# Performance work log

Hardware: AMD Instinct MI355X
Metric: run time of the kernel (lower is better)

The kernel has to match this reference:

```python
import jax, jax.numpy as jnp
import numpy as np

N = 65536
APP = 1024
SP = 512
HID = 512
CARD = 16
SUB = HID // CARD  # 32


def setup_inputs() -> dict:
    key = jax.random.key(0)
    ks = jax.random.split(key, 8)
    s1 = 1.0 / np.sqrt(APP)
    s2 = 1.0 / np.sqrt(SP)
    s3 = 1.0 / np.sqrt(SUB)
    return {
        "appearance": jax.random.normal(ks[0], (N, APP), jnp.float32),
        "spatial": jax.random.normal(ks[1], (N, SP), jnp.float32),
        # Batched per-branch weights (torch Linear: y = x @ W.T + b; here stored as [in, out])
        "W1": jax.random.uniform(ks[2], (CARD, APP, SUB), jnp.float32, -s1, s1),
        "b1": jax.random.uniform(ks[3], (CARD, SUB), jnp.float32, -s1, s1),
        "W2": jax.random.uniform(ks[4], (CARD, SP, SUB), jnp.float32, -s2, s2),
        "b2": jax.random.uniform(ks[5], (CARD, SP if False else SUB), jnp.float32, -s2, s2),
        "W3": jax.random.uniform(ks[6], (CARD, SUB, HID), jnp.float32, -s3, s3),
        "b3": jax.random.uniform(ks[7], (CARD, HID), jnp.float32, -s3, s3),
    }


def reference(appearance, spatial, W1, b1, W2, b2, W3, b3):
    # fc1[c] = appearance @ W1[c] + b1[c]; fc2[c] = spatial @ W2[c] + b2[c]
    h1 = jnp.einsum('na,cas->ncs', appearance, W1) + b1[None]  # [N, C, SUB]
    h2 = jnp.einsum('np,cps->ncs', spatial, W2) + b2[None]     # [N, C, SUB]
    h = jax.nn.relu(h1 + h2)
    # sum over branches of (h[:,c] @ W3[c] + b3[c]) == einsum + sum of biases
    out = jnp.einsum('ncs,csh->nh', h, W3) + jnp.sum(b3, axis=0)[None]  # [N, HID]
    return jax.nn.relu(out)
```

## Files before the change

### kernel.cpp

```cpp
#include <hip/hip_runtime.h>

typedef __attribute__((ext_vector_type(4))) float floatx4;
typedef __attribute__((ext_vector_type(8))) short bf16x8;

__device__ __forceinline__ unsigned short f2bf(float f) {
    union { float f; unsigned u; } v; v.f = f;
    unsigned r = v.u + 0x7fffu + ((v.u >> 16) & 1u);
    return (unsigned short)(r >> 16);
}

__global__ void prep_kernel(const float* __restrict__ W1, const float* __restrict__ b1,
                            const float* __restrict__ W2, const float* __restrict__ b2,
                            const float* __restrict__ W3, const float* __restrict__ b3,
                            unsigned short* __restrict__ wcat, unsigned short* __restrict__ w3f,
                            float* __restrict__ bias12, float* __restrict__ bias3s)
{
    int tid = blockIdx.x * 256 + threadIdx.x;
    if (tid < 98304) {
        int l  = tid & 63;
        int nt = (tid >> 6) & 31;
        int kc = tid >> 11;
        int n  = nt * 16 + (l & 15);
        int k0 = kc * 32 + ((l >> 4) << 3);
        int c = n >> 5, s = n & 31;
        union { unsigned short us[8]; int4 v; } pk;
        const float* src = (k0 < 1024) ? (W1 + c * 32768 + k0 * 32 + s)
                                       : (W2 + c * 16384 + (k0 - 1024) * 32 + s);
        #pragma unroll
        for (int j = 0; j < 8; ++j) pk.us[j] = f2bf(src[j * 32]);
        *(int4*)(wcat + (size_t)tid * 8) = pk.v;
    } else if (tid < 131072) {
        int t  = tid - 98304;
        int l  = t & 63;
        int nt = (t >> 6) & 31;
        int kc = t >> 11;
        int n  = nt * 16 + (l & 15);
        int k0 = kc * 32 + ((l >> 4) << 3);
        union { unsigned short us[8]; int4 v; } pk;
        const float* src = W3 + k0 * 512 + n;
        #pragma unroll
        for (int j = 0; j < 8; ++j) pk.us[j] = f2bf(src[j * 512]);
        *(int4*)(w3f + (size_t)t * 8) = pk.v;
    } else if (tid < 131584) {
        int n = tid - 131072;
        bias12[n] = b1[n] + b2[n];
        float sacc = 0.f;
        #pragma unroll
        for (int c = 0; c < 16; ++c) sacc += b3[c * 512 + n];
        bias3s[n] = sacc;
    }
}

__global__ __launch_bounds__(512, 4) void fused_main(
    const float* __restrict__ app, const float* __restrict__ sp,
    const unsigned short* __restrict__ wcat, const unsigned short* __restrict__ w3f,
    const float* __restrict__ bias12, const float* __restrict__ bias3s,
    float* __restrict__ out)
{
    __shared__ union {
        unsigned short As[2][2][4][64][8];
        unsigned short Hf[4][16][64][8];
    } sh;

    const int tid = (int)threadIdx.x;
    const int w   = tid >> 6;
    const int l   = tid & 63;
    const int rowbase = (int)blockIdx.x * 64;

    const int sr = tid >> 3;
    const int kq = tid & 7;
    const float* appsrc = app + (size_t)(rowbase + sr) * 1024 + kq * 8;
    const float* spsrc  = sp  + (size_t)(rowbase + sr) * 512  + kq * 8;
    unsigned short* as0 = &sh.As[0][kq >> 2][sr >> 4][(kq & 3) * 16 + (sr & 15)][0];
    unsigned short* as1 = &sh.As[1][kq >> 2][sr >> 4][(kq & 3) * 16 + (sr & 15)][0];

    floatx4 acc[4][4];
    #pragma unroll
    for (int mt = 0; mt < 4; ++mt)
        #pragma unroll
        for (int nt = 0; nt < 4; ++nt)
            acc[mt][nt] = (floatx4){0.f, 0.f, 0.f, 0.f};

    const unsigned short* wbase = wcat + (size_t)w * 2048 + (size_t)l * 8;

    bf16x8 bcur[8];
    #pragma unroll
    for (int i = 0; i < 8; ++i)
        bcur[i] = *(const bf16x8*)(wbase + (i >> 2) * 16384 + (i & 3) * 512);
    {
        float4 q0 = *(const float4*)(appsrc);
        float4 q1 = *(const float4*)(appsrc + 4);
        union { unsigned short us[8]; int4 v; } pk;
        pk.us[0] = f2bf(q0.x); pk.us[1] = f2bf(q0.y); pk.us[2] = f2bf(q0.z); pk.us[3] = f2bf(q0.w);
        pk.us[4] = f2bf(q1.x); pk.us[5] = f2bf(q1.y); pk.us[6] = f2bf(q1.z); pk.us[7] = f2bf(q1.w);
        *(int4*)as0 = pk.v;
    }
    asm volatile("s_waitcnt lgkmcnt(0)" ::: "memory");
    __builtin_amdgcn_s_barrier();

    for (int p = 0; p < 24; ++p) {
        const int buf = p & 1;
        unsigned short* dst = buf ? as0 : as1;

        float4 pA0, pA1;
        if (p + 1 < 24) {
            const float* src = (p + 1 < 16) ? (appsrc + (p + 1) * 64)
                                            : (spsrc + (p - 15) * 64);
            pA0 = *(const float4*)src;
            pA1 = *(const float4*)(src + 4);
        }

        bf16x8 af[4];
        #pragma unroll
        for (int mt = 0; mt < 4; ++mt)
            af[mt] = *(const bf16x8*)(&sh.As[buf][0][mt][l][0]);
        __builtin_amdgcn_s_setprio(1);
        #pragma unroll
        for (int mt = 0; mt < 4; ++mt)
            #pragma unroll
            for (int nt = 0; nt < 4; ++nt)
                acc[mt][nt] = __builtin_amdgcn_mfma_f32_16x16x32_bf16(
                    af[mt], bcur[nt], acc[mt][nt], 0, 0, 0);
        __builtin_amdgcn_s_setprio(0);
        #pragma unroll
        for (int mt = 0; mt < 4; ++mt)
            af[mt] = *(const bf16x8*)(&sh.As[buf][1][mt][l][0]);
        __builtin_amdgcn_s_setprio(1);
        #pragma unroll
        for (int mt = 0; mt < 4; ++mt)
            #pragma unroll
            for (int nt = 0; nt < 4; ++nt)
                acc[mt][nt] = __builtin_amdgcn_mfma_f32_16x16x32_bf16(
                    af[mt], bcur[4 + nt], acc[mt][nt], 0, 0, 0);
        __builtin_amdgcn_s_setprio(0);

        if (p + 1 < 24) {
            const unsigned short* wp = wbase + (size_t)(p + 1) * 32768;
            #pragma unroll
            for (int i = 0; i < 8; ++i)
                bcur[i] = *(const bf16x8*)(wp + (i >> 2) * 16384 + (i & 3) * 512);
            union { unsigned short us[8]; int4 v; } pk;
            pk.us[0] = f2bf(pA0.x); pk.us[1] = f2bf(pA0.y); pk.us[2] = f2bf(pA0.z); pk.us[3] = f2bf(pA0.w);
            pk.us[4] = f2bf(pA1.x); pk.us[5] = f2bf(pA1.y); pk.us[6] = f2bf(pA1.z); pk.us[7] = f2bf(pA1.w);
            *(int4*)dst = pk.v;
        }

        asm volatile("s_waitcnt lgkmcnt(0)" ::: "memory");
        __builtin_amdgcn_s_barrier();
    }

    const unsigned short* w3base = w3f + (size_t)w * 2048 + (size_t)l * 8;
    bf16x8 b3[8];
    #pragma unroll
    for (int i = 0; i < 8; ++i)
        b3[i] = *(const bf16x8*)(w3base + (i >> 2) * 16384 + (i & 3) * 512);

    #pragma unroll
    for (int nt = 0; nt < 4; ++nt) {
        const int colg = w * 64 + nt * 16 + (l & 15);
        const float bv = bias12[colg];
        const int kc  = colg >> 5;
        const int lhi = ((colg >> 3) & 3) << 4;
        const int j   = colg & 7;
        #pragma unroll
        for (int mt = 0; mt < 4; ++mt)
            #pragma unroll
            for (int r = 0; r < 4; ++r) {
                const int rlow = ((l >> 4) << 2) + r;
                float v = acc[mt][nt][r] + bv;
                v = fmaxf(v, 0.f);
                sh.Hf[mt][kc][lhi + rlow][j] = f2bf(v);
            }
    }
    asm volatile("s_waitcnt lgkmcnt(0)" ::: "memory");
    __builtin_amdgcn_s_barrier();

    #pragma unroll
    for (int mt = 0; mt < 4; ++mt)
        #pragma unroll
        for (int nt = 0; nt < 4; ++nt)
            acc[mt][nt] = (floatx4){0.f, 0.f, 0.f, 0.f};

    for (int q = 0; q < 8; ++q) {
        bf16x8 af[4];
        #pragma unroll
        for (int mt = 0; mt < 4; ++mt)
            af[mt] = *(const bf16x8*)(&sh.Hf[mt][2 * q][l][0]);
        __builtin_amdgcn_s_setprio(1);
        #pragma unroll
        for (int mt = 0; mt < 4; ++mt)
            #pragma unroll
            for (int nt = 0; nt < 4; ++nt)
                acc[mt][nt] = __builtin_amdgcn_mfma_f32_16x16x32_bf16(
                    af[mt], b3[nt], acc[mt][nt], 0, 0, 0);
        __builtin_amdgcn_s_setprio(0);
        #pragma unroll
        for (int mt = 0; mt < 4; ++mt)
            af[mt] = *(const bf16x8*)(&sh.Hf[mt][2 * q + 1][l][0]);
        __builtin_amdgcn_s_setprio(1);
        #pragma unroll
        for (int mt = 0; mt < 4; ++mt)
            #pragma unroll
            for (int nt = 0; nt < 4; ++nt)
                acc[mt][nt] = __builtin_amdgcn_mfma_f32_16x16x32_bf16(
                    af[mt], b3[4 + nt], acc[mt][nt], 0, 0, 0);
        __builtin_amdgcn_s_setprio(0);
        if (q + 1 < 8) {
            const unsigned short* wp = w3base + (size_t)(q + 1) * 32768;
            #pragma unroll
            for (int i = 0; i < 8; ++i)
                b3[i] = *(const bf16x8*)(wp + (i >> 2) * 16384 + (i & 3) * 512);
        }
    }

    #pragma unroll
    for (int nt = 0; nt < 4; ++nt) {
        const int colg = w * 64 + nt * 16 + (l & 15);
        const float bv = bias3s[colg];
        #pragma unroll
        for (int mt = 0; mt < 4; ++mt)
            #pragma unroll
            for (int r = 0; r < 4; ++r) {
                const int rowg = mt * 16 + ((l >> 4) << 2) + r;
                float v = acc[mt][nt][r] + bv;
                v = fmaxf(v, 0.f);
                out[(size_t)(rowbase + rowg) * 512 + colg] = v;
            }
    }
}

extern "C" void kernel_launch(void* const* d_in, const int* in_sizes, int n_in,
                              void* d_out, int out_size, void* d_ws, size_t ws_size,
                              hipStream_t stream)
{
    const float* app = (const float*)d_in[0];
    const float* sp  = (const float*)d_in[1];
    const float* W1  = (const float*)d_in[2];
    const float* b1  = (const float*)d_in[3];
    const float* W2  = (const float*)d_in[4];
    const float* b2  = (const float*)d_in[5];
    const float* W3  = (const float*)d_in[6];
    const float* b3  = (const float*)d_in[7];

    char* ws = (char*)d_ws;
    unsigned short* wcat  = (unsigned short*)(ws);
    unsigned short* w3f   = (unsigned short*)(ws + 1572864);
    float*          b12   = (float*)(ws + 2097152);
    float*          b3s   = (float*)(ws + 2099200);

    prep_kernel<<<514, 256, 0, stream>>>(W1, b1, W2, b2, W3, b3, wcat, w3f, b12, b3s);

    float* outp = (float*)d_out;
    fused_main<<<65536 / 64, 512, 0, stream>>>(app, sp, wcat, w3f, b12, b3s, outp);
}
```

Measured before the change: 542.8 us.

## Swizzle LDS A tile, prefetch activations two stages ahead, split weight reloads

The bf16 activation tile in shared memory gets an XOR swizzle on both its write and read addresses to cut LDS bank conflicts. Global loads of the fp32 activations now run two pipeline stages ahead instead of one, so each load has a full iteration to arrive before conversion and store. Weight register reloads are split into two halves, each issued right after the MFMA block that last used those registers, so they overlap with the remaining compute. The change adds register pressure and depends on the swizzled write and read offsets matching the original layout exactly.

```diff
diff --git a/kernel.cpp b/kernel.cpp
--- a/kernel.cpp
+++ b/kernel.cpp
@@ -71,8 +71,20 @@
     const int kq = tid & 7;
     const float* appsrc = app + (size_t)(rowbase + sr) * 1024 + kq * 8;
     const float* spsrc  = sp  + (size_t)(rowbase + sr) * 512  + kq * 8;
-    unsigned short* as0 = &sh.As[0][kq >> 2][sr >> 4][(kq & 3) * 16 + (sr & 15)][0];
-    unsigned short* as1 = &sh.As[1][kq >> 2][sr >> 4][(kq & 3) * 16 + (sr & 15)][0];
+
+    {
+    }
+    const int halfw = kq >> 2, mtw = sr >> 4;
+    const int Lw    = ((kq & 3) << 4) + (sr & 15);
+    const int roww  = Lw >> 3, slotw = Lw & 7;
+    const int wroff = halfw * 4096 + mtw * 1024 + roww * 128 + ((slotw ^ roww) << 4);
+    char* shb = (char*)&sh;
+    unsigned short* as0 = (unsigned short*)(shb + wroff);
+    unsigned short* as1 = (unsigned short*)(shb + 8192 + wroff);
+
+    const int rdoff = ((l >> 3) << 7) + (((l & 7) ^ (l >> 3)) << 4);
+    #define AS_RD(buf, half, mt) \
+        (*(const bf16x8*)(shb + (buf) * 8192 + (half) * 4096 + (mt) * 1024 + rdoff))
 
     floatx4 acc[4][4];
     #pragma unroll
@@ -83,16 +95,18 @@
 
     const unsigned short* wbase = wcat + (size_t)w * 2048 + (size_t)l * 8;
 
+    float4 c00 = *(const float4*)(appsrc);
+    float4 c01 = *(const float4*)(appsrc + 4);
+    float4 pA0 = *(const float4*)(appsrc + 64);
+    float4 pA1 = *(const float4*)(appsrc + 68);
     bf16x8 bcur[8];
     #pragma unroll
     for (int i = 0; i < 8; ++i)
         bcur[i] = *(const bf16x8*)(wbase + (i >> 2) * 16384 + (i & 3) * 512);
     {
-        float4 q0 = *(const float4*)(appsrc);
-        float4 q1 = *(const float4*)(appsrc + 4);
         union { unsigned short us[8]; int4 v; } pk;
-        pk.us[0] = f2bf(q0.x); pk.us[1] = f2bf(q0.y); pk.us[2] = f2bf(q0.z); pk.us[3] = f2bf(q0.w);
-        pk.us[4] = f2bf(q1.x); pk.us[5] = f2bf(q1.y); pk.us[6] = f2bf(q1.z); pk.us[7] = f2bf(q1.w);
+        pk.us[0] = f2bf(c00.x); pk.us[1] = f2bf(c00.y); pk.us[2] = f2bf(c00.z); pk.us[3] = f2bf(c00.w);
+        pk.us[4] = f2bf(c01.x); pk.us[5] = f2bf(c01.y); pk.us[6] = f2bf(c01.z); pk.us[7] = f2bf(c01.w);
         *(int4*)as0 = pk.v;
     }
     asm volatile("s_waitcnt lgkmcnt(0)" ::: "memory");
@@ -100,49 +114,53 @@
 
     for (int p = 0; p < 24; ++p) {
         const int buf = p & 1;
-        unsigned short* dst = buf ? as0 : as1;
-
-        float4 pA0, pA1;
+
         if (p + 1 < 24) {
-            const float* src = (p + 1 < 16) ? (appsrc + (p + 1) * 64)
-                                            : (spsrc + (p - 15) * 64);
-            pA0 = *(const float4*)src;
-            pA1 = *(const float4*)(src + 4);
-        }
-
-        bf16x8 af[4];
-        #pragma unroll
-        for (int mt = 0; mt < 4; ++mt)
-            af[mt] = *(const bf16x8*)(&sh.As[buf][0][mt][l][0]);
-        __builtin_amdgcn_s_setprio(1);
-        #pragma unroll
-        for (int mt = 0; mt < 4; ++mt)
-            #pragma unroll
-            for (int nt = 0; nt < 4; ++nt)
-                acc[mt][nt] = __builtin_amdgcn_mfma_f32_16x16x32_bf16(
-                    af[mt], bcur[nt], acc[mt][nt], 0, 0, 0);
-        __builtin_amdgcn_s_setprio(0);
-        #pragma unroll
-        for (int mt = 0; mt < 4; ++mt)
-            af[mt] = *(const bf16x8*)(&sh.As[buf][1][mt][l][0]);
-        __builtin_amdgcn_s_setprio(1);
-        #pragma unroll
-        for (int mt = 0; mt < 4; ++mt)
-            #pragma unroll
-            for (int nt = 0; nt < 4; ++nt)
-                acc[mt][nt] = __builtin_amdgcn_mfma_f32_16x16x32_bf16(
-                    af[mt], bcur[4 + nt], acc[mt][nt], 0, 0, 0);
-        __builtin_amdgcn_s_setprio(0);
-
-        if (p + 1 < 24) {
-            const unsigned short* wp = wbase + (size_t)(p + 1) * 32768;
-            #pragma unroll
-            for (int i = 0; i < 8; ++i)
-                bcur[i] = *(const bf16x8*)(wp + (i >> 2) * 16384 + (i & 3) * 512);
             union { unsigned short us[8]; int4 v; } pk;
             pk.us[0] = f2bf(pA0.x); pk.us[1] = f2bf(pA0.y); pk.us[2] = f2bf(pA0.z); pk.us[3] = f2bf(pA0.w);
             pk.us[4] = f2bf(pA1.x); pk.us[5] = f2bf(pA1.y); pk.us[6] = f2bf(pA1.z); pk.us[7] = f2bf(pA1.w);
-            *(int4*)dst = pk.v;
+            *(int4*)((buf == 0) ? as1 : as0) = pk.v;
+        }
+        if (p + 2 < 24) {
+            const int c = p + 2;
+            const float* src = (c < 16) ? (appsrc + c * 64) : (spsrc + (c - 16) * 64);
+            pA0 = *(const float4*)src;
+            pA1 = *(const float4*)(src + 4);
+        }
+
+        bf16x8 af[4];
+        #pragma unroll
+        for (int mt = 0; mt < 4; ++mt)
+            af[mt] = AS_RD(buf, 0, mt);
+        __builtin_amdgcn_s_setprio(1);
+        #pragma unroll
+        for (int mt = 0; mt < 4; ++mt)
+            #pragma unroll
+            for (int nt = 0; nt < 4; ++nt)
+                acc[mt][nt] = __builtin_amdgcn_mfma_f32_16x16x32_bf16(
+                    af[mt], bcur[nt], acc[mt][nt], 0, 0, 0);
+        __builtin_amdgcn_s_setprio(0);
+        const unsigned short* wp = wbase + (size_t)(p + 1) * 32768;
+        if (p + 1 < 24) {
+            #pragma unroll
+            for (int i = 0; i < 4; ++i)
+                bcur[i] = *(const bf16x8*)(wp + i * 512);
+        }
+        #pragma unroll
+        for (int mt = 0; mt < 4; ++mt)
+            af[mt] = AS_RD(buf, 1, mt);
+        __builtin_amdgcn_s_setprio(1);
+        #pragma unroll
+        for (int mt = 0; mt < 4; ++mt)
+            #pragma unroll
+            for (int nt = 0; nt < 4; ++nt)
+                acc[mt][nt] = __builtin_amdgcn_mfma_f32_16x16x32_bf16(
+                    af[mt], bcur[4 + nt], acc[mt][nt], 0, 0, 0);
+        __builtin_amdgcn_s_setprio(0);
+        if (p + 1 < 24) {
+            #pragma unroll
+            for (int i = 0; i < 4; ++i)
+                bcur[4 + i] = *(const bf16x8*)(wp + 16384 + i * 512);
         }
 
         asm volatile("s_waitcnt lgkmcnt(0)" ::: "memory");
@@ -227,6 +245,7 @@
                 out[(size_t)(rowbase + rowg) * 512 + colg] = v;
             }
     }
+    #undef AS_RD
 }
 
 extern "C" void kernel_launch(void* const* d_in, const int* in_sizes, int n_in,
```

Result: slower. 634.5 us (+16.9%).

## Stream fp32 activations into LDS via direct global-to-LDS loads with triple buffering

Applied to the files above, without the earlier changes.

The register-staged global load, bf16 conversion and LDS store of the activation tile is replaced by global_load_lds DMA of raw fp32 into a three-deep LDS ring. Conversion to bf16 now happens after the LDS read, just before the MFMAs. The prefetch distance becomes two periods, with vmcnt-based waits instead of lgkmcnt. This frees VGPRs and removes the per-thread store path, at the cost of double the LDS read traffic and conversion work inside the compute loop, and it depends on correct vmcnt accounting.

```diff
diff --git a/kernel.cpp b/kernel.cpp
--- a/kernel.cpp
+++ b/kernel.cpp
@@ -1,4 +1,5 @@
 #include <hip/hip_runtime.h>
+#include <hip/hip_bf16.h>
 
 typedef __attribute__((ext_vector_type(4))) float floatx4;
 typedef __attribute__((ext_vector_type(8))) short bf16x8;
@@ -7,6 +8,21 @@
     union { float f; unsigned u; } v; v.f = f;
     unsigned r = v.u + 0x7fffu + ((v.u >> 16) & 1u);
     return (unsigned short)(r >> 16);
+}
+
+__device__ __forceinline__ bf16x8 cvt8(float4 lo, float4 hi) {
+    union { __hip_bfloat16 b[8]; bf16x8 v; } u;
+    u.b[0] = __float2bfloat16(lo.x); u.b[1] = __float2bfloat16(lo.y);
+    u.b[2] = __float2bfloat16(lo.z); u.b[3] = __float2bfloat16(lo.w);
+    u.b[4] = __float2bfloat16(hi.x); u.b[5] = __float2bfloat16(hi.y);
+    u.b[6] = __float2bfloat16(hi.z); u.b[7] = __float2bfloat16(hi.w);
+    return u.v;
+}
+
+__device__ __forceinline__ void dma16(const void* gsrc, void* ldst) {
+    __builtin_amdgcn_global_load_lds(
+        (const __attribute__((address_space(1))) unsigned*)gsrc,
+        (__attribute__((address_space(3))) unsigned*)ldst, 16, 0, 0);
 }
 
 __global__ void prep_kernel(const float* __restrict__ W1, const float* __restrict__ b1,
@@ -58,21 +74,68 @@
     float* __restrict__ out)
 {
     __shared__ union {
-        unsigned short As[2][2][4][64][8];
+        float          As32[3][8][2][64][4];
         unsigned short Hf[4][16][64][8];
     } sh;
+    char* shb = (char*)&sh;
 
     const int tid = (int)threadIdx.x;
     const int w   = tid >> 6;
     const int l   = tid & 63;
     const int rowbase = (int)blockIdx.x * 64;
 
-    const int sr = tid >> 3;
-    const int kq = tid & 7;
-    const float* appsrc = app + (size_t)(rowbase + sr) * 1024 + kq * 8;
-    const float* spsrc  = sp  + (size_t)(rowbase + sr) * 512  + kq * 8;
-    unsigned short* as0 = &sh.As[0][kq >> 2][sr >> 4][(kq & 3) * 16 + (sr & 15)][0];
-    unsigned short* as1 = &sh.As[1][kq >> 2][sr >> 4][(kq & 3) * 16 + (sr & 15)][0];
+    const int half = w >> 2, mtw = w & 3;
+    const int grow = rowbase + mtw * 16 + (l & 15);
+    const char* appB = (const char*)app + (size_t)grow * 4096 + half * 128 + (l >> 4) * 32;
+    const char* spB  = (const char*)sp  + (size_t)grow * 2048 + half * 128 + (l >> 4) * 32;
+
+    #define DMA_T(t) do {                                                     \
+        const char* _g = ((t) < 16) ? (appB + (t) * 256)                      \
+                                    : (spB + ((t) - 16) * 256);               \
+        char* _d = shb + ((t) % 3) * 16384 + w * 2048;                        \
+        dma16(_g,      _d);                                                   \
+        dma16(_g + 16, _d + 1024);                                            \
+    } while (0)
+
+    #define BLOAD(kp) do {                                                    \
+        const unsigned short* _wp = wbase + (size_t)(kp) * 32768;             \
+        _Pragma("unroll")                                                     \
+        for (int i = 0; i < 8; ++i)                                           \
+            bcur[i] = *(const bf16x8*)(_wp + (i >> 2) * 16384 + (i & 3) * 512);\
+    } while (0)
+
+    #define PERIOD_CORE(p) do {                                               \
+        const int _bo = ((p) % 3) * 16384;                                    \
+        bf16x8 af[4];                                                         \
+        _Pragma("unroll")                                                     \
+        for (int mt = 0; mt < 4; ++mt) {                                      \
+            float4 lo = *(const float4*)(shb + _bo + mt * 2048 + l * 16);     \
+            float4 hi = *(const float4*)(shb + _bo + mt * 2048 + 1024 + l * 16);\
+            af[mt] = cvt8(lo, hi);                                            \
+        }                                                                     \
+        __builtin_amdgcn_s_setprio(1);                                        \
+        _Pragma("unroll")                                                     \
+        for (int mt = 0; mt < 4; ++mt)                                        \
+            _Pragma("unroll")                                                 \
+            for (int nt = 0; nt < 4; ++nt)                                    \
+                acc[mt][nt] = __builtin_amdgcn_mfma_f32_16x16x32_bf16(        \
+                    af[mt], bcur[nt], acc[mt][nt], 0, 0, 0);                  \
+        __builtin_amdgcn_s_setprio(0);                                        \
+        _Pragma("unroll")                                                     \
+        for (int mt = 0; mt < 4; ++mt) {                                      \
+            float4 lo = *(const float4*)(shb + _bo + (4 + mt) * 2048 + l * 16);\
+            float4 hi = *(const float4*)(shb + _bo + (4 + mt) * 2048 + 1024 + l * 16);\
+            af[mt] = cvt8(lo, hi);                                            \
+        }                                                                     \
+        __builtin_amdgcn_s_setprio(1);                                        \
+        _Pragma("unroll")                                                     \
+        for (int mt = 0; mt < 4; ++mt)                                        \
+            _Pragma("unroll")                                                 \
+            for (int nt = 0; nt < 4; ++nt)                                    \
+                acc[mt][nt] = __builtin_amdgcn_mfma_f32_16x16x32_bf16(        \
+                    af[mt], bcur[4 + nt], acc[mt][nt], 0, 0, 0);              \
+        __builtin_amdgcn_s_setprio(0);                                        \
+    } while (0)
 
     floatx4 acc[4][4];
     #pragma unroll
@@ -84,70 +147,29 @@
     const unsigned short* wbase = wcat + (size_t)w * 2048 + (size_t)l * 8;
 
     bf16x8 bcur[8];
-    #pragma unroll
-    for (int i = 0; i < 8; ++i)
-        bcur[i] = *(const bf16x8*)(wbase + (i >> 2) * 16384 + (i & 3) * 512);
-    {
-        float4 q0 = *(const float4*)(appsrc);
-        float4 q1 = *(const float4*)(appsrc + 4);
-        union { unsigned short us[8]; int4 v; } pk;
-        pk.us[0] = f2bf(q0.x); pk.us[1] = f2bf(q0.y); pk.us[2] = f2bf(q0.z); pk.us[3] = f2bf(q0.w);
-        pk.us[4] = f2bf(q1.x); pk.us[5] = f2bf(q1.y); pk.us[6] = f2bf(q1.z); pk.us[7] = f2bf(q1.w);
-        *(int4*)as0 = pk.v;
-    }
-    asm volatile("s_waitcnt lgkmcnt(0)" ::: "memory");
-    __builtin_amdgcn_s_barrier();
-
-    for (int p = 0; p < 24; ++p) {
-        const int buf = p & 1;
-        unsigned short* dst = buf ? as0 : as1;
-
-        float4 pA0, pA1;
-        if (p + 1 < 24) {
-            const float* src = (p + 1 < 16) ? (appsrc + (p + 1) * 64)
-                                            : (spsrc + (p - 15) * 64);
-            pA0 = *(const float4*)src;
-            pA1 = *(const float4*)(src + 4);
-        }
-
-        bf16x8 af[4];
-        #pragma unroll
-        for (int mt = 0; mt < 4; ++mt)
-            af[mt] = *(const bf16x8*)(&sh.As[buf][0][mt][l][0]);
-        __builtin_amdgcn_s_setprio(1);
-        #pragma unroll
-        for (int mt = 0; mt < 4; ++mt)
-            #pragma unroll
-            for (int nt = 0; nt < 4; ++nt)
-                acc[mt][nt] = __builtin_amdgcn_mfma_f32_16x16x32_bf16(
-                    af[mt], bcur[nt], acc[mt][nt], 0, 0, 0);
-        __builtin_amdgcn_s_setprio(0);
-        #pragma unroll
-        for (int mt = 0; mt < 4; ++mt)
-            af[mt] = *(const bf16x8*)(&sh.As[buf][1][mt][l][0]);
-        __builtin_amdgcn_s_setprio(1);
-        #pragma unroll
-        for (int mt = 0; mt < 4; ++mt)
-            #pragma unroll
-            for (int nt = 0; nt < 4; ++nt)
-                acc[mt][nt] = __builtin_amdgcn_mfma_f32_16x16x32_bf16(
-                    af[mt], bcur[4 + nt], acc[mt][nt], 0, 0, 0);
-        __builtin_amdgcn_s_setprio(0);
-
-        if (p + 1 < 24) {
-            const unsigned short* wp = wbase + (size_t)(p + 1) * 32768;
-            #pragma unroll
-            for (int i = 0; i < 8; ++i)
-                bcur[i] = *(const bf16x8*)(wp + (i >> 2) * 16384 + (i & 3) * 512);
-            union { unsigned short us[8]; int4 v; } pk;
-            pk.us[0] = f2bf(pA0.x); pk.us[1] = f2bf(pA0.y); pk.us[2] = f2bf(pA0.z); pk.us[3] = f2bf(pA0.w);
-            pk.us[4] = f2bf(pA1.x); pk.us[5] = f2bf(pA1.y); pk.us[6] = f2bf(pA1.z); pk.us[7] = f2bf(pA1.w);
-            *(int4*)dst = pk.v;
-        }
-
-        asm volatile("s_waitcnt lgkmcnt(0)" ::: "memory");
+    BLOAD(0);
+    DMA_T(0);
+    DMA_T(1);
+    asm volatile("s_waitcnt vmcnt(2)" ::: "memory");
+    __builtin_amdgcn_s_barrier();
+    asm volatile("" ::: "memory");
+
+    for (int p = 0; p < 22; ++p) {
+        PERIOD_CORE(p);
+        BLOAD(p + 1);
+        DMA_T(p + 2);
+        asm volatile("s_waitcnt vmcnt(10)" ::: "memory");
         __builtin_amdgcn_s_barrier();
-    }
+        asm volatile("" ::: "memory");
+    }
+    PERIOD_CORE(22);
+    BLOAD(23);
+    asm volatile("s_waitcnt vmcnt(8)" ::: "memory");
+    __builtin_amdgcn_s_barrier();
+    asm volatile("" ::: "memory");
+    PERIOD_CORE(23);
+    __builtin_amdgcn_s_barrier();
+    asm volatile("" ::: "memory");
 
     const unsigned short* w3base = w3f + (size_t)w * 2048 + (size_t)l * 8;
     bf16x8 b3[8];
@@ -174,6 +196,7 @@
     }
     asm volatile("s_waitcnt lgkmcnt(0)" ::: "memory");
     __builtin_amdgcn_s_barrier();
+    asm volatile("" ::: "memory");
 
     #pragma unroll
     for (int mt = 0; mt < 4; ++mt)
@@ -227,6 +250,9 @@
                 out[(size_t)(rowbase + rowg) * 512 + colg] = v;
             }
     }
+    #undef PERIOD_CORE
+    #undef BLOAD
+    #undef DMA_T
 }
 
 extern "C" void kernel_launch(void* const* d_in, const int* in_sizes, int n_in,
```

Result: slower. 627.1 us (+15.5%).
